# Kernel tuning notes

Hardware: AMD Instinct MI355X
Metric: run time of the kernel (lower is better)

The kernel has to match this reference:

```python
import jax, jax.numpy as jnp
import numpy as np

N = 100_000   # nodes
E = 200_000   # directed edges
G = 2_500     # graphs in batch
F_NODE = 16
F_EDGE = 8
H1 = 32
H2 = 16


def setup_inputs() -> dict:
    key = jax.random.key(0)
    ks = jax.random.split(key, 24)
    p = lambda k, shape: 0.1 * jax.random.normal(k, shape, dtype=jnp.float32)
    inp = {
        "x": jax.random.normal(ks[0], (N, F_NODE), dtype=jnp.float32),
        "edge_attr": jax.random.normal(ks[1], (E, F_EDGE), dtype=jnp.float32),
        # edge-MLP for conv1: F_EDGE -> 16 -> F_NODE*H1
        "w_e1a": p(ks[2], (F_EDGE, 16)), "b_e1a": p(ks[3], (16,)),
        "w_e1b": p(ks[4], (16, F_NODE * H1)), "b_e1b": p(ks[5], (F_NODE * H1,)),
        "w_root1": p(ks[6], (F_NODE, H1)), "b_root1": p(ks[7], (H1,)),
        # edge-MLP for conv2: F_EDGE -> 16 -> H1*H2
        "w_e2a": p(ks[8], (F_EDGE, 16)), "b_e2a": p(ks[9], (16,)),
        "w_e2b": p(ks[10], (16, H1 * H2)), "b_e2b": p(ks[11], (H1 * H2,)),
        "w_root2": p(ks[12], (H1, H2)), "b_root2": p(ks[13], (H2,)),
        # attention-pool gate nn: F_NODE -> F_NODE -> 1
        "w_g1": p(ks[14], (F_NODE, F_NODE)), "b_g1": p(ks[15], (F_NODE,)),
        "w_g2": p(ks[16], (F_NODE, 1)), "b_g2": p(ks[17], (1,)),
        # head: (H2 + F_NODE) -> 8 -> 1
        "w_l1": p(ks[18], (H2 + F_NODE, 8)), "b_l1": p(ks[19], (8,)),
        "w_l2": p(ks[20], (8, 1)), "b_l2": p(ks[21], (1,)),
        "edge_index": jax.random.randint(ks[22], (2, E), 0, N),
        "batch": jnp.sort(jax.random.randint(ks[23], (N,), 0, G)),
    }
    return inp


def _nnconv(x, src, tgt, edge_attr, wa, ba, wb, bb, wr, br, in_c, out_c, n):
    # PyG NNConv: x_i' = x_i @ W_root + b + sum_{j->i} x_j @ Theta(e_ji)
    h = jax.nn.relu(edge_attr @ wa + ba)              # [E, 16]
    theta = (h @ wb + bb).reshape(-1, in_c, out_c)    # [E, in, out]
    msg = jnp.einsum('ei,eio->eo', x[src], theta)     # [E, out]
    agg = jax.ops.segment_sum(msg, tgt, num_segments=n)
    return x @ wr + br + agg


def reference(x, edge_attr, w_e1a, b_e1a, w_e1b, b_e1b, w_root1, b_root1,
              w_e2a, b_e2a, w_e2b, b_e2b, w_root2, b_root2,
              w_g1, b_g1, w_g2, b_g2, w_l1, b_l1, w_l2, b_l2,
              edge_index, batch):
    src, tgt = edge_index[0], edge_index[1]
    n = x.shape[0]

    # GlobalAttention pooling on raw node features (per-graph segment softmax)
    gate = jax.nn.relu(x @ w_g1 + b_g1) @ w_g2 + b_g2          # [N, 1]
    m = jax.ops.segment_max(gate, batch, num_segments=G)       # [G, 1]
    a = jnp.exp(gate - m[batch])
    s = jax.ops.segment_sum(a, batch, num_segments=G)
    x_att = jax.ops.segment_sum((a / s[batch]) * x, batch, num_segments=G)  # [G, F_NODE]

    # Two NNConv layers with ReLU
    h = jax.nn.relu(_nnconv(x, src, tgt, edge_attr, w_e1a, b_e1a, w_e1b, b_e1b,
                            w_root1, b_root1, F_NODE, H1, n))
    h = jax.nn.relu(_nnconv(h, src, tgt, edge_attr, w_e2a, b_e2a, w_e2b, b_e2b,
                            w_root2, b_root2, H1, H2, n))

    # global_mean_pool
    cnt = jax.ops.segment_sum(jnp.ones((n, 1), h.dtype), batch, num_segments=G)
    mean = jax.ops.segment_sum(h, batch, num_segments=G) / jnp.maximum(cnt, 1.0)

    z = jnp.concatenate([mean, x_att], axis=1)  # [G, H2 + F_NODE]
    # eval mode: dropout p=0.5 is identity; two linear layers, no activation between
    z = z @ w_l1 + b_l1
    z = z @ w_l2 + b_l2
    return z
```

## Files before the change

kernel.cpp:

```cpp
#include <hip/hip_runtime.h>
#include <hip/hip_bf16.h>

#define NN 100000
#define NE 200000
#define NG 2500
#define FN 16
#define FE 8
#define H1C 32
#define H2C 16
#define KH 16

typedef __attribute__((ext_vector_type(4))) float f32x4;
typedef _Float16 __attribute__((ext_vector_type(2))) half2v;
typedef _Float16 __attribute__((ext_vector_type(8))) half8v;
typedef __fp16 __attribute__((ext_vector_type(2))) pkf16x2;

__device__ __forceinline__ float bf2f(unsigned int u){
  union { unsigned int i; float f; } v; v.i = (u & 0xffffu) << 16; return v.f;
}
__device__ __forceinline__ unsigned int pkh(float a, float b){
  union { pkf16x2 h; unsigned int u; } v; v.h = __builtin_amdgcn_cvt_pkrtz(a, b); return v.u;
}
__device__ __forceinline__ float h2lo(unsigned int u){
  union { unsigned short s; _Float16 h; } v; v.s = (unsigned short)u; return (float)v.h;
}
__device__ __forceinline__ float h2hi(unsigned int u){
  union { unsigned short s; _Float16 h; } v; v.s = (unsigned short)(u >> 16); return (float)v.h;
}
__device__ __forceinline__ float rdf(const void* p, long i, bool isbf){
  return isbf ? bf2f(((const unsigned short*)p)[i]) : ((const float*)p)[i];
}
__device__ __forceinline__ void atomic_pk_f16(unsigned short* addr, unsigned int pk){
  asm volatile("global_atomic_pk_add_f16 %0, %1, off" :: "v"(addr), "v"(pk) : "memory");
}
__device__ __forceinline__ bool detect_isbf(const void* __restrict__ x){
  const unsigned short* u = (const unsigned short*)x;
  int lane = threadIdx.x & 63;
  float f = bf2f(u[2*lane]);
  float a = fabsf(f);
  bool sane = (f == 0.0f) || (a > 1e-4f && a < 1e4f);
  unsigned long long b = __ballot(sane);
  return __popcll(b) >= 32;
}

#define NW 20
struct WArgs { const void* p[NW]; };
enum {
  OW_E1A=0,     OB_E1A=128,   OW_E1B=144,   OB_E1B=8336,  OW_R1=8848,  OB_R1=9360,
  OW_E2A=9392,  OB_E2A=9520,  OW_E2B=9536,  OB_E2B=17728, OW_R2=18240, OB_R2=18752,
  OW_G1=18768,  OB_G1=19024,  OW_G2=19040,  OB_G2=19056,
  OW_L1=19057,  OB_L1=19313,  OW_L2=19321,  OB_L2=19329
};

#define MB_A 76
#define MB_B (MB_A + 19)
#define MB_C (MB_B + 18)
#define MB_D (MB_C + 391)
#define MB_E (MB_D + 782)
#define MB_F (MB_E + 586)
__global__ void __launch_bounds__(256) mega1_kernel(
    const void* __restrict__ xin, const void* __restrict__ efin, WArgs w,
    const int* __restrict__ batch,
    float* __restrict__ wts, unsigned int* __restrict__ wpack1, unsigned int* __restrict__ wpack2,
    float* __restrict__ gate, float* __restrict__ xf,
    unsigned int* __restrict__ hpk1, unsigned int* __restrict__ hpk2,
    int* __restrict__ gstart, unsigned short* __restrict__ agg1)
{
  int b = blockIdx.x, tid = threadIdx.x;
  if(b < MB_A){
    bool isbf = detect_isbf(xin);
    int i = b*256 + tid;
    if(i >= 19330) return;
    const int sz[NW] = {128,16,8192,512,512,32, 128,16,8192,512,512,16, 256,16,16,1, 256,8,8,1};
    int seg = 0; long base = 0;
    while(i - base >= sz[seg]){ base += sz[seg]; seg++; }
    wts[i] = rdf(w.p[seg], i - base, isbf);
    return;
  }
  if(b < MB_B){
    bool isbf = detect_isbf(xin);
    int j = (b - MB_A)*256 + tid;
    if(j >= 4736) return;
    int n = j / 148; int k = (j % 148) * 2;
    float v0 = 0.f, v1 = 0.f;
    if(k < 256)        v0 = rdf(w.p[2], (long)k*32 + n, isbf);
    else if(k < 272)   v0 = rdf(w.p[3], (long)(k-256)*32 + n, isbf);
    if(k+1 < 256)      v1 = rdf(w.p[2], (long)(k+1)*32 + n, isbf);
    else if(k+1 < 272) v1 = rdf(w.p[3], (long)(k+1-256)*32 + n, isbf);
    wpack1[j] = pkh(v0, v1);
    return;
  }
  if(b < MB_C){
    bool isbf = detect_isbf(xin);
    int j = (b - MB_B)*256 + tid;
    if(j >= 4416) return;
    int n = j / 276; int k = (j % 276) * 2;
    float v0 = 0.f, v1 = 0.f;
    if(k < 512)        v0 = rdf(w.p[8], (long)k*16 + n, isbf);
    else if(k < 544)   v0 = rdf(w.p[9], (long)(k-512)*16 + n, isbf);
    if(k+1 < 512)      v1 = rdf(w.p[8], (long)(k+1)*16 + n, isbf);
    else if(k+1 < 544) v1 = rdf(w.p[9], (long)(k+1-512)*16 + n, isbf);
    wpack2[j] = pkh(v0, v1);
    return;
  }
  if(b < MB_D){
    __shared__ float s_w1[FN*FN], s_b1[FN], s_w2[FN], s_b2v[1];
    bool isbf = detect_isbf(xin);
    if(tid < FN*FN) s_w1[tid] = rdf(w.p[12], tid, isbf);
    if(tid < FN){ s_b1[tid] = rdf(w.p[13], tid, isbf); s_w2[tid] = rdf(w.p[14], tid, isbf); }
    if(tid == 0) s_b2v[0] = rdf(w.p[15], 0, isbf);
    __syncthreads();
    int n = (b - MB_C)*256 + tid;
    if(n >= NN) return;
    {
      int b1 = batch[n];
      int b0 = (n == 0) ? -1 : batch[n-1];
      for(int g2 = b0 + 1; g2 <= b1; g2++) gstart[g2] = n;
      if(n == NN-1) for(int g2 = b1 + 1; g2 <= NG; g2++) gstart[g2] = NN;
    }
    float xv[FN];
    if(isbf){
      uint4 u0 = ((const uint4*)xin)[2*n], u1 = ((const uint4*)xin)[2*n+1];
      xv[0]=bf2f(u0.x); xv[1]=bf2f(u0.x>>16); xv[2]=bf2f(u0.y); xv[3]=bf2f(u0.y>>16);
      xv[4]=bf2f(u0.z); xv[5]=bf2f(u0.z>>16); xv[6]=bf2f(u0.w); xv[7]=bf2f(u0.w>>16);
      xv[8]=bf2f(u1.x); xv[9]=bf2f(u1.x>>16); xv[10]=bf2f(u1.y); xv[11]=bf2f(u1.y>>16);
      xv[12]=bf2f(u1.z); xv[13]=bf2f(u1.z>>16); xv[14]=bf2f(u1.w); xv[15]=bf2f(u1.w>>16);
    } else {
      #pragma unroll
      for(int q = 0; q < 4; q++){
        float4 v = ((const float4*)xin)[4*n + q];
        xv[q*4+0]=v.x; xv[q*4+1]=v.y; xv[q*4+2]=v.z; xv[q*4+3]=v.w;
      }
    }
    float4* xo = (float4*)(xf + (size_t)n*FN);
    #pragma unroll
    for(int q = 0; q < 4; q++) xo[q] = make_float4(xv[q*4+0], xv[q*4+1], xv[q*4+2], xv[q*4+3]);
    float g = s_b2v[0];
    #pragma unroll
    for(int j = 0; j < FN; j++){
      float hj = s_b1[j];
      #pragma unroll
      for(int i = 0; i < FN; i++) hj += xv[i] * s_w1[i*FN + j];
      hj = hj > 0.f ? hj : 0.f;
      g += hj * s_w2[j];
    }
    gate[n] = g;
    return;
  }
  if(b < MB_E){
    __shared__ float s_w1[FE*KH], s_b1[KH], s_w2[FE*KH], s_b2[KH];
    bool isbf = detect_isbf(xin);
    if(tid < FE*KH){ s_w1[tid] = rdf(w.p[0], tid, isbf); s_w2[tid] = rdf(w.p[6], tid, isbf); }
    if(tid < KH){ s_b1[tid] = rdf(w.p[1], tid, isbf); s_b2[tid] = rdf(w.p[7], tid, isbf); }
    __syncthreads();
    int e = (b - MB_D)*256 + tid;
    if(e >= NE) return;
    float ev[FE];
    if(isbf){
      uint4 u = ((const uint4*)efin)[e];
      ev[0]=bf2f(u.x); ev[1]=bf2f(u.x>>16); ev[2]=bf2f(u.y); ev[3]=bf2f(u.y>>16);
      ev[4]=bf2f(u.z); ev[5]=bf2f(u.z>>16); ev[6]=bf2f(u.w); ev[7]=bf2f(u.w>>16);
    } else {
      float4 a = ((const float4*)efin)[2*e], bb = ((const float4*)efin)[2*e+1];
      ev[0]=a.x; ev[1]=a.y; ev[2]=a.z; ev[3]=a.w; ev[4]=bb.x; ev[5]=bb.y; ev[6]=bb.z; ev[7]=bb.w;
    }
    unsigned int o[8];
    #pragma unroll
    for(int d = 0; d < 8; d++){
      float h0 = s_b1[2*d], h1 = s_b1[2*d+1];
      #pragma unroll
      for(int k = 0; k < FE; k++){
        h0 += ev[k] * s_w1[k*KH + 2*d];
        h1 += ev[k] * s_w1[k*KH + 2*d+1];
      }
      h0 = h0 > 0.f ? h0 : 0.f; h1 = h1 > 0.f ? h1 : 0.f;
      o[d] = pkh(h0, h1);
    }
    uint4* p1 = (uint4*)(hpk1 + (size_t)e*8);
    p1[0] = make_uint4(o[0],o[1],o[2],o[3]); p1[1] = make_uint4(o[4],o[5],o[6],o[7]);
    #pragma unroll
    for(int d = 0; d < 8; d++){
      float h0 = s_b2[2*d], h1 = s_b2[2*d+1];
      #pragma unroll
      for(int k = 0; k < FE; k++){
        h0 += ev[k] * s_w2[k*KH + 2*d];
        h1 += ev[k] * s_w2[k*KH + 2*d+1];
      }
      h0 = h0 > 0.f ? h0 : 0.f; h1 = h1 > 0.f ? h1 : 0.f;
      o[d] = pkh(h0, h1);
    }
    uint4* p2 = (uint4*)(hpk2 + (size_t)e*8);
    p2[0] = make_uint4(o[0],o[1],o[2],o[3]); p2[1] = make_uint4(o[4],o[5],o[6],o[7]);
    return;
  }
  {
    int idx = (b - MB_E)*256 + tid;
    if(idx < 150000){
      uint4 z = make_uint4(0,0,0,0);
      uint4* p = (uint4*)((char*)agg1 + (size_t)idx*64);
      p[0] = z; p[1] = z; p[2] = z; p[3] = z;
    }
  }
}

#define CONV_NB (NE/64)
#define ATT_NB  (NG/4)
template<int IN, int OUT, bool AH, bool ATT>
__global__ void __launch_bounds__(256) conv_atomic_kernel(
    const void* __restrict__ nodef, const unsigned int* __restrict__ hpk,
    const int* __restrict__ ei, const unsigned short* __restrict__ wpack,
    unsigned short* __restrict__ agg,
    const float* __restrict__ gate, const float* __restrict__ xf,
    const int* __restrict__ gstart, float* __restrict__ xatt)
{
  if(ATT && blockIdx.x >= CONV_NB){
    int lane = threadIdx.x & 63, wid = threadIdx.x >> 6;
    int g = (blockIdx.x - CONV_NB)*4 + wid;
    int start = gstart[g], end = gstart[g+1];
    float mx = -1e30f;
    for(int n = start + lane; n < end; n += 64) mx = fmaxf(mx, gate[n]);
    #pragma unroll
    for(int o = 32; o >= 1; o >>= 1) mx = fmaxf(mx, __shfl_xor(mx, o));
    float s = 0.f;
    float acc[FN];
    #pragma unroll
    for(int f = 0; f < FN; f++) acc[f] = 0.f;
    for(int n = start + lane; n < end; n += 64){
      float a = __expf(gate[n] - mx);
      s += a;
      const float4* xp = (const float4*)(xf + (size_t)n * FN);
      #pragma unroll
      for(int q = 0; q < 4; q++){
        float4 v = xp[q];
        acc[q*4+0] += a*v.x; acc[q*4+1] += a*v.y; acc[q*4+2] += a*v.z; acc[q*4+3] += a*v.w;
      }
    }
    #pragma unroll
    for(int o = 32; o >= 1; o >>= 1){
      s += __shfl_xor(s, o);
      #pragma unroll
      for(int f = 0; f < FN; f++) acc[f] += __shfl_xor(acc[f], o);
    }
    if(lane < FN) xatt[(size_t)g*FN + lane] = (end > start && s > 0.f) ? acc[lane] / s : 0.f;
    return;
  }
  constexpr int KMF  = ((KH*IN + IN + 31)/32)*32;
  constexpr int KP   = KMF + 8;
  constexpr int NT   = OUT/16;
  constexpr int KS   = KMF/32;
  int tid = threadIdx.x;
  int lane = tid & 63, m = lane & 15, quad = lane >> 4;
  int wid = tid >> 6;
  int ebase = blockIdx.x*64 + wid*16;
  int em = ebase + m;
  int sn = ei[em];
  int q1 = quad >> 1;
  int xoff = (IN == 16) ? ((quad & 1)*8) : (quad*8);
  union { half8v v; half2v h[4]; unsigned int w[4]; } X;
  if(AH){
    uint4 u = *(const uint4*)((const unsigned short*)nodef + (size_t)sn*IN + xoff);
    X.w[0]=u.x; X.w[1]=u.y; X.w[2]=u.z; X.w[3]=u.w;
  } else {
    const float4* xp = (const float4*)((const float*)nodef + (size_t)sn*IN + xoff);
    float4 v0 = xp[0], v1 = xp[1];
    X.w[0] = pkh(v0.x, v0.y);
    X.w[1] = pkh(v0.z, v0.w);
    X.w[2] = pkh(v1.x, v1.y);
    X.w[3] = pkh(v1.z, v1.w);
  }
  unsigned int hu[8];
  {
    const uint4* hp = (const uint4*)(hpk + (size_t)em*8);
    uint4 u0 = hp[0], u1 = hp[1];
    hu[0]=u0.x; hu[1]=u0.y; hu[2]=u0.z; hu[3]=u0.w;
    hu[4]=u1.x; hu[5]=u1.y; hu[6]=u1.z; hu[7]=u1.w;
  }
  int4 tg = *(const int4*)(ei + NE + ebase + quad*4);

  f32x4 acc[NT];
  #pragma unroll
  for(int nt = 0; nt < NT; nt++) acc[nt] = (f32x4){0.f,0.f,0.f,0.f};

  const half8v hz = {};
  #pragma unroll
  for(int ks = 0; ks < KS; ks++){
    union { half8v v; half2v h[4]; } A;
    if(ks < KS-1){
      unsigned short hs = (unsigned short)((IN == 16) ? (hu[ks] >> (16*q1))
                                                      : (hu[ks >> 1] >> (16*(ks & 1))));
      union { unsigned short s; _Float16 h; } hc; hc.s = hs;
      half2v hv2 = { hc.h, hc.h };
      #pragma unroll
      for(int k = 0; k < 4; k++) A.h[k] = hv2 * X.h[k];
    } else {
      if(IN == 16) A.v = (quad < 2) ? X.v : hz;
      else         A.v = X.v;
    }
    #pragma unroll
    for(int nt = 0; nt < NT; nt++){
      half8v b = *(const half8v*)(wpack + (size_t)(nt*16 + m)*KP + ks*32 + quad*8);
      acc[nt] = __builtin_amdgcn_mfma_f32_16x16x32_f16(A.v, b, acc[nt], 0, 0, 0);
    }
  }
  int tr[4] = {tg.x, tg.y, tg.z, tg.w};
  int mlo = m & ~1;
  bool evn = (m & 1) == 0;
  #pragma unroll
  for(int r = 0; r < 4; r++){
    #pragma unroll
    for(int nt = 0; nt < NT; nt++){
      float v = acc[nt][r];
      float vn = __shfl_xor(v, 1);
      if(evn ? (r < 2) : (r >= 2)){
        unsigned int pk = evn ? pkh(v, vn) : pkh(vn, v);
        atomic_pk_f16(agg + (size_t)tr[r]*OUT + nt*16 + mlo, pk);
      }
    }
  }
}

__global__ void __launch_bounds__(256) node1_kernel(
    const float* __restrict__ xf, const unsigned short* __restrict__ agg1,
    const float* __restrict__ wr, const float* __restrict__ br,
    unsigned short* __restrict__ h1b)
{
  __shared__ float s_w[FN*H1C], s_b[H1C];
  for(int i = threadIdx.x; i < FN*H1C; i += 256) s_w[i] = wr[i];
  if(threadIdx.x < H1C) s_b[threadIdx.x] = br[threadIdx.x];
  __syncthreads();
  int g = blockIdx.x*256 + threadIdx.x;
  int n = g >> 3, q = g & 7;
  if(n >= NN) return;
  uint2 au = *(const uint2*)(agg1 + (size_t)n*H1C + q*4);
  float a0 = s_b[q*4+0] + h2lo(au.x), a1 = s_b[q*4+1] + h2hi(au.x);
  float a2 = s_b[q*4+2] + h2lo(au.y), a3 = s_b[q*4+3] + h2hi(au.y);
  const float* xr = xf + (size_t)n*FN;
  #pragma unroll
  for(int i = 0; i < FN; i++){
    float xi = xr[i];
    a0 += xi*s_w[i*H1C + q*4+0]; a1 += xi*s_w[i*H1C + q*4+1];
    a2 += xi*s_w[i*H1C + q*4+2]; a3 += xi*s_w[i*H1C + q*4+3];
  }
  a0 = a0>0.f?a0:0.f; a1 = a1>0.f?a1:0.f; a2 = a2>0.f?a2:0.f; a3 = a3>0.f?a3:0.f;
  uint2 hb; hb.x = pkh(a0, a1); hb.y = pkh(a2, a3);
  *(uint2*)(h1b + (size_t)n*H1C + q*4) = hb;
}

__global__ void __launch_bounds__(256) node2_kernel(
    const unsigned short* __restrict__ h1b, const unsigned short* __restrict__ agg2,
    const float* __restrict__ wr, const float* __restrict__ br, float* __restrict__ h2)
{
  __shared__ float s_w[H1C*H2C], s_b[H2C];
  for(int i = threadIdx.x; i < H1C*H2C; i += 256) s_w[i] = wr[i];
  if(threadIdx.x < H2C) s_b[threadIdx.x] = br[threadIdx.x];
  __syncthreads();
  int g = blockIdx.x*256 + threadIdx.x;
  int n = g >> 2, q = g & 3;
  if(n >= NN) return;
  uint2 au = *(const uint2*)(agg2 + (size_t)n*H2C + q*4);
  float a0 = s_b[q*4+0] + h2lo(au.x), a1 = s_b[q*4+1] + h2hi(au.x);
  float a2 = s_b[q*4+2] + h2lo(au.y), a3 = s_b[q*4+3] + h2hi(au.y);
  const unsigned int* hb = (const unsigned int*)(h1b + (size_t)n*H1C);
  #pragma unroll
  for(int i2 = 0; i2 < H1C/2; i2++){
    unsigned int u = hb[i2];
    float x0 = h2lo(u), x1 = h2hi(u);
    int i = 2*i2;
    a0 += x0*s_w[i*H2C + q*4+0] + x1*s_w[(i+1)*H2C + q*4+0];
    a1 += x0*s_w[i*H2C + q*4+1] + x1*s_w[(i+1)*H2C + q*4+1];
    a2 += x0*s_w[i*H2C + q*4+2] + x1*s_w[(i+1)*H2C + q*4+2];
    a3 += x0*s_w[i*H2C + q*4+3] + x1*s_w[(i+1)*H2C + q*4+3];
  }
  float4 r; r.x = a0>0.f?a0:0.f; r.y = a1>0.f?a1:0.f; r.z = a2>0.f?a2:0.f; r.w = a3>0.f?a3:0.f;
  *(float4*)(h2 + (size_t)n*H2C + q*4) = r;
}

__global__ void head_kernel(const float* __restrict__ xatt,
    const float* __restrict__ h2, const int* __restrict__ gstart, const void* __restrict__ xin,
    const float* __restrict__ wl1, const float* __restrict__ bl1,
    const float* __restrict__ wl2, const float* __restrict__ bl2,
    void* __restrict__ out)
{
  __shared__ float sz[H2C + FN];
  int g = blockIdx.x;
  int lane = threadIdx.x;
  bool isbf = detect_isbf(xin);
  int start = gstart[g];
  int end   = gstart[g + 1];
  float acc[H2C];
  #pragma unroll
  for(int f = 0; f < H2C; f++) acc[f] = 0.f;
  for(int n = start + lane; n < end; n += 64){
    const float4* hp = (const float4*)(h2 + (size_t)n*H2C);
    #pragma unroll
    for(int q = 0; q < 4; q++){
      float4 v = hp[q];
      acc[q*4+0] += v.x; acc[q*4+1] += v.y; acc[q*4+2] += v.z; acc[q*4+3] += v.w;
    }
  }
  #pragma unroll
  for(int o = 32; o >= 1; o >>= 1){
    #pragma unroll
    for(int f = 0; f < H2C; f++) acc[f] += __shfl_xor(acc[f], o);
  }
  float inv = 1.f / fmaxf((float)(end - start), 1.f);
  if(lane < H2C) sz[lane] = acc[lane] * inv;
  if(lane < FN)  sz[H2C + lane] = xatt[(size_t)g*FN + lane];
  __syncthreads();
  if(lane == 0){
    float t1[8];
    #pragma unroll
    for(int j = 0; j < 8; j++){
      float t = bl1[j];
      #pragma unroll
      for(int c = 0; c < H2C + FN; c++) t += sz[c] * wl1[c*8 + j];
      t1[j] = t;
    }
    float o = bl2[0];
    #pragma unroll
    for(int j = 0; j < 8; j++) o += t1[j] * wl2[j];
    if(isbf) ((__hip_bfloat16*)out)[g] = __float2bfloat16(o);
    else     ((float*)out)[g] = o;
  }
}

extern "C" void kernel_launch(void* const* d_in, const int* in_sizes, int n_in,
                              void* d_out, int out_size, void* d_ws, size_t ws_size,
                              hipStream_t stream)
{
  const int* ei    = (const int*)d_in[22];
  const int* batch = (const int*)d_in[23];

  float* ws = (float*)d_ws;
  float* xf     = ws;
  float* gate   = xf + 1600000;
  float* wts    = gate + 100000;
  float* xatt   = wts + 19360;
  int*   gstart = (int*)(xatt + 40000);
  unsigned int* wpack1 = (unsigned int*)(gstart + 2504);
  unsigned int* wpack2 = wpack1 + 4736;
  unsigned int* hpk1   = wpack2 + 4416;
  unsigned int* hpk2   = hpk1 + 1600000;
  unsigned short* h1b  = (unsigned short*)(hpk2 + 1600000);
  float* h2     = (float*)(h1b + 3200000);
  unsigned short* agg1 = (unsigned short*)(h2 + 1600000);
  unsigned short* agg2 = agg1 + 3200000;

  WArgs wa;
  for(int i = 0; i < NW; i++) wa.p[i] = d_in[2 + i];

  mega1_kernel<<<MB_F, 256, 0, stream>>>(d_in[0], d_in[1], wa, batch,
      wts, wpack1, wpack2, gate, xf, hpk1, hpk2, gstart, agg1);

  conv_atomic_kernel<FN, H1C, false, true><<<CONV_NB + ATT_NB, 256, 0, stream>>>(
      xf, hpk1, ei, (const unsigned short*)wpack1, agg1, gate, xf, gstart, xatt);
  node1_kernel<<<(NN*8 + 255)/256, 256, 0, stream>>>(xf, agg1, wts+OW_R1, wts+OB_R1, h1b);

  conv_atomic_kernel<H1C, H2C, true, false><<<CONV_NB, 256, 0, stream>>>(
      h1b, hpk2, ei, (const unsigned short*)wpack2, agg2, gate, xf, gstart, xatt);
  node2_kernel<<<(NN*4 + 255)/256, 256, 0, stream>>>(h1b, agg2, wts+OW_R2, wts+OB_R2, h2);

  head_kernel<<<NG, 64, 0, stream>>>(xatt, h2, gstart, d_in[0],
      wts+OW_L1, wts+OB_L1, wts+OW_L2, wts+OB_L2, d_out);
}
```

Before: 186.8 us.

## Drop fp32 node-feature copy and move conv2 edge-MLP into conv1 launch

Removes the intermediate fp32 copy of the node features. The gate, attention-pool, conv1 gather and node1 root paths now read the raw input directly through a shared load helper. The conv2 edge-MLP hidden computation and the agg2 zeroing move out of the first mega kernel into the conv1 launch, running beside the conv tiles and attention blocks. This saves a write and several re-reads of a 6.4MB buffer and shortens the serial first kernel. In exchange it repeats bf16/fp32 conversion at each read and adds block-type branching to conv1.

```diff
diff --git a/kernel.cpp b/kernel.cpp
--- a/kernel.cpp
+++ b/kernel.cpp
@@ -42,6 +42,21 @@
   unsigned long long b = __ballot(sane);
   return __popcll(b) >= 32;
 }
+__device__ __forceinline__ void load_x16(const void* __restrict__ xin, bool isbf, int n, float* xv){
+  if(isbf){
+    uint4 u0 = ((const uint4*)xin)[2*n], u1 = ((const uint4*)xin)[2*n+1];
+    xv[0]=bf2f(u0.x); xv[1]=bf2f(u0.x>>16); xv[2]=bf2f(u0.y); xv[3]=bf2f(u0.y>>16);
+    xv[4]=bf2f(u0.z); xv[5]=bf2f(u0.z>>16); xv[6]=bf2f(u0.w); xv[7]=bf2f(u0.w>>16);
+    xv[8]=bf2f(u1.x); xv[9]=bf2f(u1.x>>16); xv[10]=bf2f(u1.y); xv[11]=bf2f(u1.y>>16);
+    xv[12]=bf2f(u1.z); xv[13]=bf2f(u1.z>>16); xv[14]=bf2f(u1.w); xv[15]=bf2f(u1.w>>16);
+  } else {
+    #pragma unroll
+    for(int q = 0; q < 4; q++){
+      float4 v = ((const float4*)xin)[4*n + q];
+      xv[q*4+0]=v.x; xv[q*4+1]=v.y; xv[q*4+2]=v.z; xv[q*4+3]=v.w;
+    }
+  }
+}
 
 #define NW 20
 struct WArgs { const void* p[NW]; };
@@ -52,18 +67,107 @@
   OW_L1=19057,  OB_L1=19313,  OW_L2=19321,  OB_L2=19329
 };
 
+template<int IN, int OUT, bool RAWX>
+__device__ __forceinline__ void conv_tile(
+    int u, const void* __restrict__ nodef, bool isbf,
+    const unsigned int* __restrict__ hpk, const int* __restrict__ ei,
+    const unsigned short* __restrict__ wpack, unsigned short* __restrict__ agg)
+{
+  constexpr int KMF  = ((KH*IN + IN + 31)/32)*32;
+  constexpr int KP   = KMF + 8;
+  constexpr int NT   = OUT/16;
+  constexpr int KS   = KMF/32;
+  int tid = threadIdx.x;
+  int lane = tid & 63, m = lane & 15, quad = lane >> 4;
+  int wid = tid >> 6;
+  int ebase = u*64 + wid*16;
+  int em = ebase + m;
+  int sn = ei[em];
+  int q1 = quad >> 1;
+  int xoff = (IN == 16) ? ((quad & 1)*8) : (quad*8);
+  union { half8v v; half2v h[4]; unsigned int w[4]; } X;
+  if(RAWX){
+    if(isbf){
+      uint4 uu = *(const uint4*)((const unsigned short*)nodef + (size_t)sn*IN + xoff);
+      X.w[0] = pkh(bf2f(uu.x), bf2f(uu.x >> 16));
+      X.w[1] = pkh(bf2f(uu.y), bf2f(uu.y >> 16));
+      X.w[2] = pkh(bf2f(uu.z), bf2f(uu.z >> 16));
+      X.w[3] = pkh(bf2f(uu.w), bf2f(uu.w >> 16));
+    } else {
+      const float4* xp = (const float4*)((const float*)nodef + (size_t)sn*IN + xoff);
+      float4 v0 = xp[0], v1 = xp[1];
+      X.w[0] = pkh(v0.x, v0.y);
+      X.w[1] = pkh(v0.z, v0.w);
+      X.w[2] = pkh(v1.x, v1.y);
+      X.w[3] = pkh(v1.z, v1.w);
+    }
+  } else {
+    uint4 uu = *(const uint4*)((const unsigned short*)nodef + (size_t)sn*IN + xoff);
+    X.w[0]=uu.x; X.w[1]=uu.y; X.w[2]=uu.z; X.w[3]=uu.w;
+  }
+  unsigned int hu[8];
+  {
+    const uint4* hp = (const uint4*)(hpk + (size_t)em*8);
+    uint4 u0 = hp[0], u1 = hp[1];
+    hu[0]=u0.x; hu[1]=u0.y; hu[2]=u0.z; hu[3]=u0.w;
+    hu[4]=u1.x; hu[5]=u1.y; hu[6]=u1.z; hu[7]=u1.w;
+  }
+  int4 tg = *(const int4*)(ei + NE + ebase + quad*4);
+
+  f32x4 acc[NT];
+  #pragma unroll
+  for(int nt = 0; nt < NT; nt++) acc[nt] = (f32x4){0.f,0.f,0.f,0.f};
+
+  const half8v hz = {};
+  #pragma unroll
+  for(int ks = 0; ks < KS; ks++){
+    union { half8v v; half2v h[4]; } A;
+    if(ks < KS-1){
+      unsigned short hs = (unsigned short)((IN == 16) ? (hu[ks] >> (16*q1))
+                                                      : (hu[ks >> 1] >> (16*(ks & 1))));
+      union { unsigned short s; _Float16 h; } hc; hc.s = hs;
+      half2v hv2 = { hc.h, hc.h };
+      #pragma unroll
+      for(int k = 0; k < 4; k++) A.h[k] = hv2 * X.h[k];
+    } else {
+      if(IN == 16) A.v = (quad < 2) ? X.v : hz;
+      else         A.v = X.v;
+    }
+    #pragma unroll
+    for(int nt = 0; nt < NT; nt++){
+      half8v b = *(const half8v*)(wpack + (size_t)(nt*16 + m)*KP + ks*32 + quad*8);
+      acc[nt] = __builtin_amdgcn_mfma_f32_16x16x32_f16(A.v, b, acc[nt], 0, 0, 0);
+    }
+  }
+  int tr[4] = {tg.x, tg.y, tg.z, tg.w};
+  int mlo = m & ~1;
+  bool evn = (m & 1) == 0;
+  #pragma unroll
+  for(int r = 0; r < 4; r++){
+    #pragma unroll
+    for(int nt = 0; nt < NT; nt++){
+      float v = acc[nt][r];
+      float vn = __shfl_xor(v, 1);
+      if(evn ? (r < 2) : (r >= 2)){
+        unsigned int pk = evn ? pkh(v, vn) : pkh(vn, v);
+        atomic_pk_f16(agg + (size_t)tr[r]*OUT + nt*16 + mlo, pk);
+      }
+    }
+  }
+}
+
 #define MB_A 76
 #define MB_B (MB_A + 19)
 #define MB_C (MB_B + 18)
 #define MB_D (MB_C + 391)
 #define MB_E (MB_D + 782)
-#define MB_F (MB_E + 586)
+#define MB_F (MB_E + 391)
 __global__ void __launch_bounds__(256) mega1_kernel(
     const void* __restrict__ xin, const void* __restrict__ efin, WArgs w,
     const int* __restrict__ batch,
     float* __restrict__ wts, unsigned int* __restrict__ wpack1, unsigned int* __restrict__ wpack2,
-    float* __restrict__ gate, float* __restrict__ xf,
-    unsigned int* __restrict__ hpk1, unsigned int* __restrict__ hpk2,
+    float* __restrict__ gate,
+    unsigned int* __restrict__ hpk1,
     int* __restrict__ gstart, unsigned short* __restrict__ agg1)
 {
   int b = blockIdx.x, tid = threadIdx.x;
@@ -119,22 +223,7 @@
       if(n == NN-1) for(int g2 = b1 + 1; g2 <= NG; g2++) gstart[g2] = NN;
     }
     float xv[FN];
-    if(isbf){
-      uint4 u0 = ((const uint4*)xin)[2*n], u1 = ((const uint4*)xin)[2*n+1];
-      xv[0]=bf2f(u0.x); xv[1]=bf2f(u0.x>>16); xv[2]=bf2f(u0.y); xv[3]=bf2f(u0.y>>16);
-      xv[4]=bf2f(u0.z); xv[5]=bf2f(u0.z>>16); xv[6]=bf2f(u0.w); xv[7]=bf2f(u0.w>>16);
-      xv[8]=bf2f(u1.x); xv[9]=bf2f(u1.x>>16); xv[10]=bf2f(u1.y); xv[11]=bf2f(u1.y>>16);
-      xv[12]=bf2f(u1.z); xv[13]=bf2f(u1.z>>16); xv[14]=bf2f(u1.w); xv[15]=bf2f(u1.w>>16);
-    } else {
-      #pragma unroll
-      for(int q = 0; q < 4; q++){
-        float4 v = ((const float4*)xin)[4*n + q];
-        xv[q*4+0]=v.x; xv[q*4+1]=v.y; xv[q*4+2]=v.z; xv[q*4+3]=v.w;
-      }
-    }
-    float4* xo = (float4*)(xf + (size_t)n*FN);
-    #pragma unroll
-    for(int q = 0; q < 4; q++) xo[q] = make_float4(xv[q*4+0], xv[q*4+1], xv[q*4+2], xv[q*4+3]);
+    load_x16(xin, isbf, n, xv);
     float g = s_b2v[0];
     #pragma unroll
     for(int j = 0; j < FN; j++){
@@ -148,10 +237,10 @@
     return;
   }
   if(b < MB_E){
-    __shared__ float s_w1[FE*KH], s_b1[KH], s_w2[FE*KH], s_b2[KH];
+    __shared__ float s_w1[FE*KH], s_b1[KH];
     bool isbf = detect_isbf(xin);
-    if(tid < FE*KH){ s_w1[tid] = rdf(w.p[0], tid, isbf); s_w2[tid] = rdf(w.p[6], tid, isbf); }
-    if(tid < KH){ s_b1[tid] = rdf(w.p[1], tid, isbf); s_b2[tid] = rdf(w.p[7], tid, isbf); }
+    if(tid < FE*KH) s_w1[tid] = rdf(w.p[0], tid, isbf);
+    if(tid < KH) s_b1[tid] = rdf(w.p[1], tid, isbf);
     __syncthreads();
     int e = (b - MB_D)*256 + tid;
     if(e >= NE) return;
@@ -178,6 +267,55 @@
     }
     uint4* p1 = (uint4*)(hpk1 + (size_t)e*8);
     p1[0] = make_uint4(o[0],o[1],o[2],o[3]); p1[1] = make_uint4(o[4],o[5],o[6],o[7]);
+    return;
+  }
+  {
+    int idx = (b - MB_E)*256 + tid;
+    if(idx < 100000){
+      uint4 z = make_uint4(0,0,0,0);
+      uint4* p = (uint4*)((char*)agg1 + (size_t)idx*64);
+      p[0] = z; p[1] = z; p[2] = z; p[3] = z;
+    }
+  }
+}
+
+#define C1_CONV (NE/64)
+#define C1_E2   (C1_CONV + 782)
+#define C1_Z    (C1_E2 + 196)
+#define C1_ATT  (C1_Z + 625)
+__global__ void __launch_bounds__(256) conv1_kernel(
+    const void* __restrict__ xin, const void* __restrict__ efin,
+    const float* __restrict__ wts,
+    const unsigned int* __restrict__ hpk1, const int* __restrict__ ei,
+    const unsigned short* __restrict__ wpack1,
+    unsigned short* __restrict__ agg1, unsigned short* __restrict__ agg2,
+    unsigned int* __restrict__ hpk2,
+    const float* __restrict__ gate, const int* __restrict__ gstart,
+    float* __restrict__ xatt)
+{
+  int b = blockIdx.x, tid = threadIdx.x;
+  bool isbf = detect_isbf(xin);
+  if(b < C1_CONV){
+    conv_tile<FN, H1C, true>(b, xin, isbf, hpk1, ei, wpack1, agg1);
+    return;
+  }
+  if(b < C1_E2){
+    __shared__ float s_w2[FE*KH], s_b2[KH];
+    if(tid < FE*KH) s_w2[tid] = wts[OW_E2A + tid];
+    if(tid < KH) s_b2[tid] = wts[OB_E2A + tid];
+    __syncthreads();
+    int e = (b - C1_CONV)*256 + tid;
+    if(e >= NE) return;
+    float ev[FE];
+    if(isbf){
+      uint4 u = ((const uint4*)efin)[e];
+      ev[0]=bf2f(u.x); ev[1]=bf2f(u.x>>16); ev[2]=bf2f(u.y); ev[3]=bf2f(u.y>>16);
+      ev[4]=bf2f(u.z); ev[5]=bf2f(u.z>>16); ev[6]=bf2f(u.w); ev[7]=bf2f(u.w>>16);
+    } else {
+      float4 a = ((const float4*)efin)[2*e], bb = ((const float4*)efin)[2*e+1];
+      ev[0]=a.x; ev[1]=a.y; ev[2]=a.z; ev[3]=a.w; ev[4]=bb.x; ev[5]=bb.y; ev[6]=bb.z; ev[7]=bb.w;
+    }
+    unsigned int o[8];
     #pragma unroll
     for(int d = 0; d < 8; d++){
       float h0 = s_b2[2*d], h1 = s_b2[2*d+1];
@@ -193,29 +331,18 @@
     p2[0] = make_uint4(o[0],o[1],o[2],o[3]); p2[1] = make_uint4(o[4],o[5],o[6],o[7]);
     return;
   }
+  if(b < C1_Z){
+    int idx = (b - C1_E2)*256 + tid;
+    if(idx < 50000){
+      uint4 z = make_uint4(0,0,0,0);
+      uint4* p = (uint4*)((char*)agg2 + (size_t)idx*64);
+      p[0] = z; p[1] = z; p[2] = z; p[3] = z;
+    }
+    return;
+  }
   {
-    int idx = (b - MB_E)*256 + tid;
-    if(idx < 150000){
-      uint4 z = make_uint4(0,0,0,0);
-      uint4* p = (uint4*)((char*)agg1 + (size_t)idx*64);
-      p[0] = z; p[1] = z; p[2] = z; p[3] = z;
-    }
-  }
-}
-
-#define CONV_NB (NE/64)
-#define ATT_NB  (NG/4)
-template<int IN, int OUT, bool AH, bool ATT>
-__global__ void __launch_bounds__(256) conv_atomic_kernel(
-    const void* __restrict__ nodef, const unsigned int* __restrict__ hpk,
-    const int* __restrict__ ei, const unsigned short* __restrict__ wpack,
-    unsigned short* __restrict__ agg,
-    const float* __restrict__ gate, const float* __restrict__ xf,
-    const int* __restrict__ gstart, float* __restrict__ xatt)
-{
-  if(ATT && blockIdx.x >= CONV_NB){
-    int lane = threadIdx.x & 63, wid = threadIdx.x >> 6;
-    int g = (blockIdx.x - CONV_NB)*4 + wid;
+    int lane = tid & 63, wid = tid >> 6;
+    int g = (b - C1_Z)*4 + wid;
     int start = gstart[g], end = gstart[g+1];
     float mx = -1e30f;
     for(int n = start + lane; n < end; n += 64) mx = fmaxf(mx, gate[n]);
@@ -228,12 +355,10 @@
     for(int n = start + lane; n < end; n += 64){
       float a = __expf(gate[n] - mx);
       s += a;
-      const float4* xp = (const float4*)(xf + (size_t)n * FN);
-      #pragma unroll
-      for(int q = 0; q < 4; q++){
-        float4 v = xp[q];
-        acc[q*4+0] += a*v.x; acc[q*4+1] += a*v.y; acc[q*4+2] += a*v.z; acc[q*4+3] += a*v.w;
-      }
+      float xv[FN];
+      load_x16(xin, isbf, n, xv);
+      #pragma unroll
+      for(int f = 0; f < FN; f++) acc[f] += a * xv[f];
     }
     #pragma unroll
     for(int o = 32; o >= 1; o >>= 1){
@@ -242,91 +367,26 @@
       for(int f = 0; f < FN; f++) acc[f] += __shfl_xor(acc[f], o);
     }
     if(lane < FN) xatt[(size_t)g*FN + lane] = (end > start && s > 0.f) ? acc[lane] / s : 0.f;
-    return;
-  }
-  constexpr int KMF  = ((KH*IN + IN + 31)/32)*32;
-  constexpr int KP   = KMF + 8;
-  constexpr int NT   = OUT/16;
-  constexpr int KS   = KMF/32;
-  int tid = threadIdx.x;
-  int lane = tid & 63, m = lane & 15, quad = lane >> 4;
-  int wid = tid >> 6;
-  int ebase = blockIdx.x*64 + wid*16;
-  int em = ebase + m;
-  int sn = ei[em];
-  int q1 = quad >> 1;
-  int xoff = (IN == 16) ? ((quad & 1)*8) : (quad*8);
-  union { half8v v; half2v h[4]; unsigned int w[4]; } X;
-  if(AH){
-    uint4 u = *(const uint4*)((const unsigned short*)nodef + (size_t)sn*IN + xoff);
-    X.w[0]=u.x; X.w[1]=u.y; X.w[2]=u.z; X.w[3]=u.w;
-  } else {
-    const float4* xp = (const float4*)((const float*)nodef + (size_t)sn*IN + xoff);
-    float4 v0 = xp[0], v1 = xp[1];
-    X.w[0] = pkh(v0.x, v0.y);
-    X.w[1] = pkh(v0.z, v0.w);
-    X.w[2] = pkh(v1.x, v1.y);
-    X.w[3] = pkh(v1.z, v1.w);
-  }
-  unsigned int hu[8];
-  {
-    const uint4* hp = (const uint4*)(hpk + (size_t)em*8);
-    uint4 u0 = hp[0], u1 = hp[1];
-    hu[0]=u0.x; hu[1]=u0.y; hu[2]=u0.z; hu[3]=u0.w;
-    hu[4]=u1.x; hu[5]=u1.y; hu[6]=u1.z; hu[7]=u1.w;
-  }
-  int4 tg = *(const int4*)(ei + NE + ebase + quad*4);
-
-  f32x4 acc[NT];
-  #pragma unroll
-  for(int nt = 0; nt < NT; nt++) acc[nt] = (f32x4){0.f,0.f,0.f,0.f};
-
-  const half8v hz = {};
-  #pragma unroll
-  for(int ks = 0; ks < KS; ks++){
-    union { half8v v; half2v h[4]; } A;
-    if(ks < KS-1){
-      unsigned short hs = (unsigned short)((IN == 16) ? (hu[ks] >> (16*q1))
-                                                      : (hu[ks >> 1] >> (16*(ks & 1))));
-      union { unsigned short s; _Float16 h; } hc; hc.s = hs;
-      half2v hv2 = { hc.h, hc.h };
-      #pragma unroll
-      for(int k = 0; k < 4; k++) A.h[k] = hv2 * X.h[k];
-    } else {
-      if(IN == 16) A.v = (quad < 2) ? X.v : hz;
-      else         A.v = X.v;
-    }
-    #pragma unroll
-    for(int nt = 0; nt < NT; nt++){
-      half8v b = *(const half8v*)(wpack + (size_t)(nt*16 + m)*KP + ks*32 + quad*8);
-      acc[nt] = __builtin_amdgcn_mfma_f32_16x16x32_f16(A.v, b, acc[nt], 0, 0, 0);
-    }
-  }
-  int tr[4] = {tg.x, tg.y, tg.z, tg.w};
-  int mlo = m & ~1;
-  bool evn = (m & 1) == 0;
-  #pragma unroll
-  for(int r = 0; r < 4; r++){
-    #pragma unroll
-    for(int nt = 0; nt < NT; nt++){
-      float v = acc[nt][r];
-      float vn = __shfl_xor(v, 1);
-      if(evn ? (r < 2) : (r >= 2)){
-        unsigned int pk = evn ? pkh(v, vn) : pkh(vn, v);
-        atomic_pk_f16(agg + (size_t)tr[r]*OUT + nt*16 + mlo, pk);
-      }
-    }
-  }
+  }
+}
+
+__global__ void __launch_bounds__(256) conv2_kernel(
+    const unsigned short* __restrict__ h1b, const unsigned int* __restrict__ hpk2,
+    const int* __restrict__ ei, const unsigned short* __restrict__ wpack2,
+    unsigned short* __restrict__ agg2)
+{
+  conv_tile<H1C, H2C, false>(blockIdx.x, h1b, false, hpk2, ei, wpack2, agg2);
 }
 
 __global__ void __launch_bounds__(256) node1_kernel(
-    const float* __restrict__ xf, const unsigned short* __restrict__ agg1,
+    const void* __restrict__ xin, const unsigned short* __restrict__ agg1,
     const float* __restrict__ wr, const float* __restrict__ br,
     unsigned short* __restrict__ h1b)
 {
   __shared__ float s_w[FN*H1C], s_b[H1C];
   for(int i = threadIdx.x; i < FN*H1C; i += 256) s_w[i] = wr[i];
   if(threadIdx.x < H1C) s_b[threadIdx.x] = br[threadIdx.x];
+  bool isbf = detect_isbf(xin);
   __syncthreads();
   int g = blockIdx.x*256 + threadIdx.x;
   int n = g >> 3, q = g & 7;
@@ -334,10 +394,11 @@
   uint2 au = *(const uint2*)(agg1 + (size_t)n*H1C + q*4);
   float a0 = s_b[q*4+0] + h2lo(au.x), a1 = s_b[q*4+1] + h2hi(au.x);
   float a2 = s_b[q*4+2] + h2lo(au.y), a3 = s_b[q*4+3] + h2hi(au.y);
-  const float* xr = xf + (size_t)n*FN;
+  float xv[FN];
+  load_x16(xin, isbf, n, xv);
   #pragma unroll
   for(int i = 0; i < FN; i++){
-    float xi = xr[i];
+    float xi = xv[i];
     a0 += xi*s_w[i*H1C + q*4+0]; a1 += xi*s_w[i*H1C + q*4+1];
     a2 += xi*s_w[i*H1C + q*4+2]; a3 += xi*s_w[i*H1C + q*4+3];
   }
@@ -432,8 +493,7 @@
   const int* batch = (const int*)d_in[23];
 
   float* ws = (float*)d_ws;
-  float* xf     = ws;
-  float* gate   = xf + 1600000;
+  float* gate   = ws;
   float* wts    = gate + 100000;
   float* xatt   = wts + 19360;
   int*   gstart = (int*)(xatt + 40000);
@@ -450,14 +510,14 @@
   for(int i = 0; i < NW; i++) wa.p[i] = d_in[2 + i];
 
   mega1_kernel<<<MB_F, 256, 0, stream>>>(d_in[0], d_in[1], wa, batch,
-      wts, wpack1, wpack2, gate, xf, hpk1, hpk2, gstart, agg1);
-
-  conv_atomic_kernel<FN, H1C, false, true><<<CONV_NB + ATT_NB, 256, 0, stream>>>(
-      xf, hpk1, ei, (const unsigned short*)wpack1, agg1, gate, xf, gstart, xatt);
-  node1_kernel<<<(NN*8 + 255)/256, 256, 0, stream>>>(xf, agg1, wts+OW_R1, wts+OB_R1, h1b);
-
-  conv_atomic_kernel<H1C, H2C, true, false><<<CONV_NB, 256, 0, stream>>>(
-      h1b, hpk2, ei, (const unsigned short*)wpack2, agg2, gate, xf, gstart, xatt);
+      wts, wpack1, wpack2, gate, hpk1, gstart, agg1);
+
+  conv1_kernel<<<C1_ATT, 256, 0, stream>>>(d_in[0], d_in[1], wts, hpk1, ei,
+      (const unsigned short*)wpack1, agg1, agg2, hpk2, gate, gstart, xatt);
+  node1_kernel<<<(NN*8 + 255)/256, 256, 0, stream>>>(d_in[0], agg1, wts+OW_R1, wts+OB_R1, h1b);
+
+  conv2_kernel<<<NE/64, 256, 0, stream>>>(h1b, hpk2, ei,
+      (const unsigned short*)wpack2, agg2);
   node2_kernel<<<(NN*4 + 255)/256, 256, 0, stream>>>(h1b, agg2, wts+OW_R2, wts+OB_R2, h2);
 
   head_kernel<<<NG, 64, 0, stream>>>(xatt, h2, gstart, d_in[0],
```

Result: no change. 185.0 us (-1.0%).
